# Kernel optimization log

Measured on AMD Instinct MI355X. Metric: run time of the kernel, lower is better.

The kernel has to match this reference:

```python
import jax, jax.numpy as jnp
import numpy as np

B, N, H = 32, 2048, 128


def _lstm_step(c, h, x, Wi, Wh, b):
    # flax LSTMCell: gates i,f,g,o; sigmoid/sigmoid/tanh/sigmoid
    gates = x @ Wi + h @ Wh + b  # (B,N,4H)
    i, f, g, o = jnp.split(gates, 4, axis=-1)
    c_new = jax.nn.sigmoid(f) * c + jax.nn.sigmoid(i) * jnp.tanh(g)
    h_new = jax.nn.sigmoid(o) * jnp.tanh(c_new)
    return c_new, h_new


def setup_inputs() -> dict:
    key = jax.random.key(0)
    ks = jax.random.split(key, 24)
    f32 = jnp.float32
    inp = {}
    inp['node_embeddings'] = jax.random.normal(ks[0], (B, N, H), f32)
    for nm, k in zip(['hs_c0', 'hs_h0', 'hs_c1', 'hs_h1'], ks[1:5]):
        inp[nm] = jax.random.normal(k, (B, N, H), f32)
    ip = jax.random.uniform(ks[5], (B, N), f32)
    inp['instruction_pointer'] = ip / jnp.sum(ip, axis=-1, keepdims=True)
    inp['Wi0'] = jax.random.normal(ks[6], (H, 4 * H), f32) * 0.05
    inp['Wh0'] = jax.random.normal(ks[7], (H, 4 * H), f32) * 0.05
    inp['b0'] = jnp.zeros((4 * H,), f32)
    inp['Wi1'] = jax.random.normal(ks[8], (H, 4 * H), f32) * 0.05
    inp['Wh1'] = jax.random.normal(ks[9], (H, 4 * H), f32) * 0.05
    inp['b1'] = jnp.zeros((4 * H,), f32)
    inp['W_raise'] = jax.random.normal(ks[10], (4 * H, 2), f32) * 0.05
    inp['b_raise'] = jnp.zeros((2,), f32)
    inp['W_branch'] = jax.random.normal(ks[11], (4 * H, 2), f32) * 0.05
    inp['b_branch'] = jnp.zeros((2,), f32)
    inp['true_indexes'] = jax.random.randint(ks[12], (B, N), 0, N, jnp.int32)
    inp['false_indexes'] = jax.random.randint(ks[13], (B, N), 0, N, jnp.int32)
    inp['raise_indexes'] = jax.random.randint(ks[14], (B, N), 0, N, jnp.int32)
    inp['exit_node_indexes'] = jax.random.randint(ks[15], (B,), 0, N, jnp.int32)
    inp['raise_node_indexes'] = jax.random.randint(ks[16], (B,), 0, N, jnp.int32)
    inp['step_limits'] = jax.random.randint(ks[17], (B,), 0, 100, jnp.int32)
    inp['current_step'] = 5
    return inp


def reference(node_embeddings, hs_c0, hs_h0, hs_c1, hs_h1, instruction_pointer,
              Wi0, Wh0, b0, Wi1, Wh1, b1, W_raise, b_raise, W_branch, b_branch,
              true_indexes, false_indexes, raise_indexes,
              exit_node_indexes, raise_node_indexes, step_limits, current_step):
    bidx = jnp.arange(B)
    old = [hs_c0, hs_h0, hs_c1, hs_h1]

    # execute: per-node 2-layer stacked LSTM (vectorized over B,N)
    c0n, h0n = _lstm_step(hs_c0, hs_h0, node_embeddings, Wi0, Wh0, b0)
    c1n, h1n = _lstm_step(hs_c1, hs_h1, h0n, Wi1, Wh1, b1)
    contrib = [c0n, h0n, c1n, h1n]

    # mask_h: keep old state at exit node and (raise_in_ipagnn) at raise node
    def mask_nodes(hc, ho, idx):
        return hc.at[bidx, idx].set(ho[bidx, idx])
    contrib = [mask_nodes(mask_nodes(hc, ho, exit_node_indexes), ho, raise_node_indexes)
               for hc, ho in zip(contrib, old)]

    hs_emb = jnp.concatenate(contrib, axis=-1)  # (B,N,4H)

    raise_dec = jax.nn.softmax(hs_emb @ W_raise + b_raise, axis=-1)
    zero_one = jnp.array([0.0, 1.0], dtype=raise_dec.dtype)
    raise_dec = raise_dec.at[bidx, exit_node_indexes].set(zero_one)
    raise_dec = raise_dec.at[bidx, raise_node_indexes].set(zero_one)
    branch_dec = jax.nn.softmax(hs_emb @ W_branch + b_branch, axis=-1)

    p_raise = raise_dec[..., 0]
    p_noraise = raise_dec[..., 1]
    p_true = p_noraise * branch_dec[..., 0]
    p_false = p_noraise * branch_dec[..., 1]

    seg = jax.vmap(lambda v, idx: jax.ops.segment_sum(v, idx, num_segments=N))
    ip = instruction_pointer
    ip_new = (seg(p_raise * ip, raise_indexes)
              + seg(p_true * ip, true_indexes)
              + seg(p_false * ip, false_indexes))  # (B,N)
    denom = (ip_new + 1e-7)[..., None]

    wr = (p_raise * ip)[..., None]
    wt = (p_true * ip)[..., None]
    wf = (p_false * ip)[..., None]

    def agg(h):
        return (seg(h * wr, raise_indexes) + seg(h * wt, true_indexes)
                + seg(h * wf, false_indexes)) / denom
    hs_new = [agg(h) for h in contrib]

    # keep_old_if_done
    not_done = (current_step < step_limits)  # (B,)
    hs_out = [jnp.where(not_done[:, None, None], hn, ho) for hn, ho in zip(hs_new, old)]
    ip_out = jnp.where(not_done[:, None], ip_new, ip)

    # pack carry: (c0,h0,c1,h1, instruction_pointer) -> (B,N,4H+1)
    return jnp.concatenate(hs_out + [ip_out[..., None]], axis=-1)
```

## Files before the change

### kernel.cpp

```cpp
#include <hip/hip_runtime.h>
#include <stdint.h>

#define BB 32
#define NN 2048
#define HH 128
#define BN (BB*NN)

typedef short v8s __attribute__((ext_vector_type(8)));
typedef float v4f __attribute__((ext_vector_type(4)));

__device__ __forceinline__ unsigned short f2b(float f){
  union { float f; unsigned int i; } v; v.f = f;
  unsigned int x = v.i;
  unsigned int r = x + 0x7FFFu + ((x >> 16) & 1u);
  return (unsigned short)(r >> 16);
}
__device__ __forceinline__ unsigned int pk2(float a, float b){
  return (unsigned int)f2b(a) | ((unsigned int)f2b(b) << 16);
}
__device__ __forceinline__ float b2f(unsigned int s){
  union { unsigned int i; float f; } v; v.i = s << 16; return v.f;
}
__device__ __forceinline__ float frcp(float x){ return __builtin_amdgcn_rcpf(x); }
__device__ __forceinline__ float fsigm(float x){ return frcp(1.0f + __expf(-x)); }
__device__ __forceinline__ float ftanh(float x){ return 1.0f - 2.0f*frcp(1.0f + __expf(2.0f*x)); }

__global__ void kswz(const float* __restrict__ Wi0, const float* __restrict__ Wh0,
                     const float* __restrict__ Wi1, const float* __restrict__ Wh1,
                     unsigned short* __restrict__ Bsw0, unsigned short* __restrict__ Bsw1){
  int bid = blockIdx.x;
  int layer = bid >> 8;
  int kc = (bid >> 5) & 7;
  int ct = bid & 31;
  int lane = threadIdx.x;
  const float* Wi = layer ? Wi1 : Wi0;
  const float* Wh = layer ? Wh1 : Wh0;
  unsigned short* dst = layer ? Bsw1 : Bsw0;
  int col = ct*16 + (lane & 15);
  int kbase = kc*32 + (lane >> 4)*8;
  size_t o = ((size_t)(kc*32 + ct)*64 + (size_t)lane)*8;
  #pragma unroll
  for (int j = 0; j < 8; j++){
    int k = kbase + j;
    dst[o + j] = f2b((k < 128) ? Wi[k*512 + col] : Wh[(k-128)*512 + col]);
  }
}

#define ROWSB 32
#define PA 264
#define PH 136

__global__ __launch_bounds__(512, 4) void klstm2(
    const float* __restrict__ ne,
    float* __restrict__ c0, float* __restrict__ h0,
    float* __restrict__ c1, float* __restrict__ h1,
    unsigned short* __restrict__ sc0, unsigned short* __restrict__ sh0,
    unsigned short* __restrict__ sc1, unsigned short* __restrict__ sh1,
    const unsigned short* __restrict__ Bsw0, const float* __restrict__ b0,
    const unsigned short* __restrict__ Bsw1, const float* __restrict__ b1,
    const int* __restrict__ exit_idx, const int* __restrict__ raise_idx,
    const int* __restrict__ step_limits, const int* __restrict__ cur_step,
    int useb)
{
  __shared__ unsigned short ldsA[ROWSB*PA];
  __shared__ unsigned short ldsH[ROWSB*PH];
  __shared__ unsigned short ldsG[ROWSB*PH];

  int rowbase = blockIdx.x * ROWSB;
  int b = rowbase >> 11;
  if (cur_step[0] >= step_limits[b]) return;

  int tid = threadIdx.x;
  int wid = tid >> 6, lane = tid & 63;
  int quad = lane >> 4, l16 = lane & 15;
  int ch = wid*16 + l16;
  int e_row = exit_idx[b], r_row = raise_idx[b];

  #pragma unroll
  for (int p = 0; p < 4; p++){
    int idx = p*512 + tid;
    int row = idx >> 6, chunk = idx & 63;
    size_t g = (size_t)(rowbase + row)*128 + (chunk & 31)*4;
    float4 v = (chunk < 32) ? *(const float4*)(ne + g) : *(const float4*)(h0 + g);
    uint2 w; w.x = pk2(v.x, v.y); w.y = pk2(v.z, v.w);
    *(uint2*)&ldsA[row*PA + chunk*4] = w;
  }
  __syncthreads();

  float cpre[8], bias[4];
  #pragma unroll
  for (int rt = 0; rt < 2; rt++)
    #pragma unroll
    for (int r = 0; r < 4; r++)
      cpre[rt*4+r] = c0[((size_t)rowbase + rt*16 + quad*4 + r)*128 + ch];
  #pragma unroll
  for (int g = 0; g < 4; g++) bias[g] = b0[g*128 + ch];

  #pragma unroll
  for (int p = 0; p < 2; p++){
    int idx = p*512 + tid;
    int row = idx >> 5, chunk = idx & 31;
    float4 v = *(const float4*)(h1 + (size_t)(rowbase + row)*128 + chunk*4);
    uint2 w; w.x = pk2(v.x, v.y); w.y = pk2(v.z, v.w);
    *(uint2*)&ldsH[row*PH + chunk*4] = w;
  }

  const v8s* Bv0 = (const v8s*)Bsw0;
  v4f acc[2][4] = {};
  v8s bc[4], bn[4];
  #pragma unroll
  for (int g = 0; g < 4; g++) bc[g] = Bv0[(size_t)(g*8 + wid)*64 + lane];
  #pragma unroll
  for (int kc = 0; kc < 8; kc++){
    if (kc < 7){
      #pragma unroll
      for (int g = 0; g < 4; g++) bn[g] = Bv0[(size_t)((kc+1)*32 + g*8 + wid)*64 + lane];
    }
    v8s a0 = *(const v8s*)&ldsA[(0*16 + l16)*PA + kc*32 + quad*8];
    v8s a1 = *(const v8s*)&ldsA[(1*16 + l16)*PA + kc*32 + quad*8];
    #pragma unroll
    for (int g = 0; g < 4; g++){
      acc[0][g] = __builtin_amdgcn_mfma_f32_16x16x32_bf16(a0, bc[g], acc[0][g], 0,0,0);
      acc[1][g] = __builtin_amdgcn_mfma_f32_16x16x32_bf16(a1, bc[g], acc[1][g], 0,0,0);
    }
    #pragma unroll
    for (int g = 0; g < 4; g++) bc[g] = bn[g];
  }

  #pragma unroll
  for (int rt = 0; rt < 2; rt++){
    #pragma unroll
    for (int r = 0; r < 4; r++){
      int k = rt*4 + r;
      int lrow = rt*16 + quad*4 + r;
      int grow = rowbase + lrow;
      int node = grow & 2047;
      bool special = (node == e_row) || (node == r_row);
      float iv = acc[rt][0][r] + bias[0];
      float fv = acc[rt][1][r] + bias[1];
      float gv = acc[rt][2][r] + bias[2];
      float ov = acc[rt][3][r] + bias[3];
      float cn = fsigm(fv)*cpre[k] + fsigm(iv)*ftanh(gv);
      float hn = fsigm(ov)*ftanh(cn);
      if (useb){
        sc0[(size_t)grow*128 + ch] = special ? f2b(cpre[k]) : f2b(cn);
        sh0[(size_t)grow*128 + ch] = special ? ldsA[lrow*PA + 128 + ch] : f2b(hn);
      } else if (!special){
        c0[(size_t)grow*128 + ch] = cn;
        h0[(size_t)grow*128 + ch] = hn;
      }
      ldsG[lrow*PH + ch] = f2b(hn);
    }
  }

  #pragma unroll
  for (int rt = 0; rt < 2; rt++)
    #pragma unroll
    for (int r = 0; r < 4; r++)
      cpre[rt*4+r] = c1[((size_t)rowbase + rt*16 + quad*4 + r)*128 + ch];
  #pragma unroll
  for (int g = 0; g < 4; g++) bias[g] = b1[g*128 + ch];
  const v8s* Bv1 = (const v8s*)Bsw1;
  #pragma unroll
  for (int g = 0; g < 4; g++) bc[g] = Bv1[(size_t)(g*8 + wid)*64 + lane];

  __syncthreads();

  #pragma unroll
  for (int rt = 0; rt < 2; rt++)
    #pragma unroll
    for (int g = 0; g < 4; g++)
      acc[rt][g] = (v4f){0.f, 0.f, 0.f, 0.f};
  #pragma unroll
  for (int kc = 0; kc < 8; kc++){
    if (kc < 7){
      #pragma unroll
      for (int g = 0; g < 4; g++) bn[g] = Bv1[(size_t)((kc+1)*32 + g*8 + wid)*64 + lane];
    }
    v8s a0, a1;
    if (kc < 4){
      a0 = *(const v8s*)&ldsG[(0*16 + l16)*PH + kc*32 + quad*8];
      a1 = *(const v8s*)&ldsG[(1*16 + l16)*PH + kc*32 + quad*8];
    } else {
      a0 = *(const v8s*)&ldsH[(0*16 + l16)*PH + (kc-4)*32 + quad*8];
      a1 = *(const v8s*)&ldsH[(1*16 + l16)*PH + (kc-4)*32 + quad*8];
    }
    #pragma unroll
    for (int g = 0; g < 4; g++){
      acc[0][g] = __builtin_amdgcn_mfma_f32_16x16x32_bf16(a0, bc[g], acc[0][g], 0,0,0);
      acc[1][g] = __builtin_amdgcn_mfma_f32_16x16x32_bf16(a1, bc[g], acc[1][g], 0,0,0);
    }
    #pragma unroll
    for (int g = 0; g < 4; g++) bc[g] = bn[g];
  }

  #pragma unroll
  for (int rt = 0; rt < 2; rt++){
    #pragma unroll
    for (int r = 0; r < 4; r++){
      int k = rt*4 + r;
      int lrow = rt*16 + quad*4 + r;
      int grow = rowbase + lrow;
      int node = grow & 2047;
      bool special = (node == e_row) || (node == r_row);
      float iv = acc[rt][0][r] + bias[0];
      float fv = acc[rt][1][r] + bias[1];
      float gv = acc[rt][2][r] + bias[2];
      float ov = acc[rt][3][r] + bias[3];
      float cn = fsigm(fv)*cpre[k] + fsigm(iv)*ftanh(gv);
      float hn = fsigm(ov)*ftanh(cn);
      if (useb){
        sc1[(size_t)grow*128 + ch] = special ? f2b(cpre[k]) : f2b(cn);
        sh1[(size_t)grow*128 + ch] = special ? ldsH[lrow*PH + ch] : f2b(hn);
      } else if (!special){
        c1[(size_t)grow*128 + ch] = cn;
        h1[(size_t)grow*128 + ch] = hn;
      }
    }
  }
}

__global__ __launch_bounds__(256) void kdec(
    const float* __restrict__ c0, const float* __restrict__ h0,
    const float* __restrict__ c1, const float* __restrict__ h1,
    const unsigned short* __restrict__ sc0, const unsigned short* __restrict__ sh0,
    const unsigned short* __restrict__ sc1, const unsigned short* __restrict__ sh1,
    const float* __restrict__ Wr, const float* __restrict__ br,
    const float* __restrict__ Wb, const float* __restrict__ bb,
    const float* __restrict__ ip,
    const int* __restrict__ exit_idx, const int* __restrict__ raise_idx,
    const int* __restrict__ ri, const int* __restrict__ ti, const int* __restrict__ fi,
    int* __restrict__ counts,
    float* __restrict__ wbuf, int useb)
{
  int tid = threadIdx.x;
  int wid = tid >> 6, lane = tid & 63;
  int gid = blockIdx.x*4 + wid;
  int b = gid >> 11, n = gid & 2047;

  float hv[8];
  if (useb){
    const unsigned short* bufs16[4] = {sc0, sh0, sc1, sh1};
    const unsigned short* hb = bufs16[lane >> 4] + (size_t)gid*128 + (lane & 15)*8;
    uint4 raw = *(const uint4*)hb;
    hv[0] = b2f(raw.x & 0xffffu); hv[1] = b2f(raw.x >> 16);
    hv[2] = b2f(raw.y & 0xffffu); hv[3] = b2f(raw.y >> 16);
    hv[4] = b2f(raw.z & 0xffffu); hv[5] = b2f(raw.z >> 16);
    hv[6] = b2f(raw.w & 0xffffu); hv[7] = b2f(raw.w >> 16);
  } else {
    const float* bufs[4] = {c0, h0, c1, h1};
    const float* hb = bufs[lane >> 4] + (size_t)gid*128 + (lane & 15)*8;
    float4 hv0 = *(const float4*)hb;
    float4 hv1 = *(const float4*)(hb + 4);
    hv[0]=hv0.x; hv[1]=hv0.y; hv[2]=hv0.z; hv[3]=hv0.w;
    hv[4]=hv1.x; hv[5]=hv1.y; hv[6]=hv1.z; hv[7]=hv1.w;
  }
  const float* wrp = Wr + lane*16;
  const float* wbp = Wb + lane*16;
  float r0=0.f, r1=0.f, q0=0.f, q1=0.f;
  #pragma unroll
  for (int j = 0; j < 8; j++){
    float h = hv[j];
    r0 += h * wrp[j*2];  r1 += h * wrp[j*2+1];
    q0 += h * wbp[j*2];  q1 += h * wbp[j*2+1];
  }
  #pragma unroll
  for (int off = 32; off > 0; off >>= 1){
    r0 += __shfl_xor(r0, off, 64);
    r1 += __shfl_xor(r1, off, 64);
    q0 += __shfl_xor(q0, off, 64);
    q1 += __shfl_xor(q1, off, 64);
  }
  if (lane == 0){
    r0 += br[0]; r1 += br[1];
    q0 += bb[0]; q1 += bb[1];
    float pr, pn;
    if (n == exit_idx[b] || n == raise_idx[b]){ pr = 0.f; pn = 1.f; }
    else {
      float m = fmaxf(r0, r1);
      float e0 = __expf(r0 - m), e1 = __expf(r1 - m);
      pr = e0 / (e0 + e1); pn = e1 / (e0 + e1);
    }
    float m2 = fmaxf(q0, q1);
    float f0 = __expf(q0 - m2), f1 = __expf(q1 - m2);
    float pt = f0 / (f0 + f1), pf = f1 / (f0 + f1);
    float ipv = ip[gid];
    wbuf[0*BN + gid] = pr * ipv;
    wbuf[1*BN + gid] = pn * pt * ipv;
    wbuf[2*BN + gid] = pn * pf * ipv;
  } else if (lane == 1){
    atomicAdd(&counts[(b<<11) + ri[gid]], 1);
  } else if (lane == 2){
    atomicAdd(&counts[(b<<11) + ti[gid]], 1);
  } else if (lane == 3){
    atomicAdd(&counts[(b<<11) + fi[gid]], 1);
  }
}

__global__ __launch_bounds__(256) void kscan(const int* __restrict__ counts,
                                             int* __restrict__ offsets,
                                             int* __restrict__ cursor){
  __shared__ int lds[256];
  int b = blockIdx.x, tid = threadIdx.x;
  const int* c = counts + b*NN;
  int* o = offsets + b*NN;
  int* cu = cursor + b*NN;
  int v[8]; int s = 0;
  #pragma unroll
  for (int i = 0; i < 8; i++){ v[i] = c[tid*8+i]; s += v[i]; cu[tid*8+i] = 0; }
  lds[tid] = s;
  __syncthreads();
  if (tid == 0){
    int run = 0;
    for (int t = 0; t < 256; t++){ int tmp = lds[t]; lds[t] = run; run += tmp; }
  }
  __syncthreads();
  int off = lds[tid];
  #pragma unroll
  for (int i = 0; i < 8; i++){ o[tid*8+i] = off; off += v[i]; }
}

__global__ void kfill(const int* __restrict__ ri, const int* __restrict__ ti,
                      const int* __restrict__ fi, const int* __restrict__ offsets,
                      int* __restrict__ cursor, unsigned short* __restrict__ edges){
  int gid = blockIdx.x*256 + threadIdx.x;
  int b = gid >> 11, n = gid & 2047;
  size_t ebase = (size_t)b*3*NN;
  int t0 = ri[gid]; int p0 = atomicAdd(&cursor[b*NN+t0], 1);
  edges[ebase + offsets[b*NN+t0] + p0] = (unsigned short)(n);
  int t1 = ti[gid]; int p1 = atomicAdd(&cursor[b*NN+t1], 1);
  edges[ebase + offsets[b*NN+t1] + p1] = (unsigned short)(n | (1<<11));
  int t2 = fi[gid]; int p2 = atomicAdd(&cursor[b*NN+t2], 1);
  edges[ebase + offsets[b*NN+t2] + p2] = (unsigned short)(n | (2<<11));
}

__global__ __launch_bounds__(128) void kagg(
    const float* __restrict__ c0, const float* __restrict__ h0,
    const float* __restrict__ c1, const float* __restrict__ h1,
    const unsigned short* __restrict__ sc0, const unsigned short* __restrict__ sh0,
    const unsigned short* __restrict__ sc1, const unsigned short* __restrict__ sh1,
    const float* __restrict__ ip,
    const float* __restrict__ wbuf, const unsigned short* __restrict__ edges,
    const int* __restrict__ counts, const int* __restrict__ offsets,
    const int* __restrict__ step_limits, const int* __restrict__ cur_step,
    float* __restrict__ out, int useb)
{
  int gid = blockIdx.x;
  int b = gid >> 11;
  int tid = threadIdx.x;
  size_t obase = (size_t)gid*513;
  const float* bufs[4] = {c0, h0, c1, h1};

  if (cur_step[0] >= step_limits[b]){
    int c = tid*4;
    const float* s = bufs[c >> 7];
    size_t rb = (size_t)gid*128 + (c & 127);
    out[obase + c+0] = s[rb+0];
    out[obase + c+1] = s[rb+1];
    out[obase + c+2] = s[rb+2];
    out[obase + c+3] = s[rb+3];
    if (tid == 0) out[obase + 512] = ip[gid];
    return;
  }

  int cnt = counts[gid], off = offsets[gid];
  const unsigned short* eb = edges + (size_t)b*3*NN + off;
  int coff = (tid & 31)*4;
  float a0=0.f, a1=0.f, a2=0.f, a3=0.f, ipn=0.f;
  int pk = (cnt > 0) ? eb[0] : 0;
  if (useb){
    const unsigned short* bufs16[4] = {sc0, sh0, sc1, sh1};
    const unsigned short* sb = bufs16[tid >> 5];
    for (int e = 0; e < cnt; e++){
      int pkn = (e+1 < cnt) ? eb[e+1] : 0;
      int n = pk & 2047, et = pk >> 11;
      float w = wbuf[et*BN + (b<<11) + n];
      uint2 raw = *(const uint2*)(sb + ((size_t)(b<<11) + n)*128 + coff);
      ipn += w;
      a0 += w * b2f(raw.x & 0xffffu);
      a1 += w * b2f(raw.x >> 16);
      a2 += w * b2f(raw.y & 0xffffu);
      a3 += w * b2f(raw.y >> 16);
      pk = pkn;
    }
  } else {
    const float* sb = bufs[tid >> 5];
    for (int e = 0; e < cnt; e++){
      int pkn = (e+1 < cnt) ? eb[e+1] : 0;
      int n = pk & 2047, et = pk >> 11;
      float w = wbuf[et*BN + (b<<11) + n];
      float4 sv = *(const float4*)(sb + ((size_t)(b<<11) + n)*128 + coff);
      ipn += w;
      a0 += w * sv.x;
      a1 += w * sv.y;
      a2 += w * sv.z;
      a3 += w * sv.w;
      pk = pkn;
    }
  }
  int c = tid*4;
  float inv = 1.0f / (ipn + 1e-7f);
  out[obase + c+0] = a0*inv;
  out[obase + c+1] = a1*inv;
  out[obase + c+2] = a2*inv;
  out[obase + c+3] = a3*inv;
  if (tid == 0) out[obase + 512] = ipn;
}

extern "C" void kernel_launch(void* const* d_in, const int* in_sizes, int n_in,
                              void* d_out, int out_size, void* d_ws, size_t ws_size,
                              hipStream_t stream){
  const float* ne  = (const float*)d_in[0];
  float* c0  = (float*)d_in[1];
  float* h0  = (float*)d_in[2];
  float* c1  = (float*)d_in[3];
  float* h1  = (float*)d_in[4];
  const float* ip  = (const float*)d_in[5];
  const float* Wi0 = (const float*)d_in[6];
  const float* Wh0 = (const float*)d_in[7];
  const float* b0  = (const float*)d_in[8];
  const float* Wi1 = (const float*)d_in[9];
  const float* Wh1 = (const float*)d_in[10];
  const float* b1  = (const float*)d_in[11];
  const float* Wr  = (const float*)d_in[12];
  const float* br  = (const float*)d_in[13];
  const float* Wb  = (const float*)d_in[14];
  const float* bb  = (const float*)d_in[15];
  const int* ti  = (const int*)d_in[16];
  const int* fi  = (const int*)d_in[17];
  const int* ri  = (const int*)d_in[18];
  const int* ei  = (const int*)d_in[19];
  const int* rni = (const int*)d_in[20];
  const int* sl  = (const int*)d_in[21];
  const int* cs  = (const int*)d_in[22];
  float* out = (float*)d_out;

  uint8_t* ws = (uint8_t*)d_ws;
  unsigned short* Bsw0    = (unsigned short*)(ws + 0);
  unsigned short* Bsw1    = (unsigned short*)(ws + 262144);
  float*          wbuf    = (float*)(ws + 655360);
  int*            counts  = (int*)(ws + 1441792);
  int*            offsets = (int*)(ws + 1703936);
  int*            cursor  = (int*)(ws + 1966080);
  unsigned short* edges   = (unsigned short*)(ws + 2228224);
  const size_t SBASE = 2621440;
  const size_t SB    = (size_t)BN * 128 * 2;
  int useb = (ws_size >= SBASE + 4*SB) ? 1 : 0;
  unsigned short* sc0 = (unsigned short*)(ws + SBASE + 0*SB);
  unsigned short* sh0 = (unsigned short*)(ws + SBASE + 1*SB);
  unsigned short* sc1 = (unsigned short*)(ws + SBASE + 2*SB);
  unsigned short* sh1 = (unsigned short*)(ws + SBASE + 3*SB);

  hipMemsetAsync(counts, 0, BN*sizeof(int), stream);

  kswz<<<512, 64, 0, stream>>>(Wi0, Wh0, Wi1, Wh1, Bsw0, Bsw1);

  klstm2<<<BN/ROWSB, 512, 0, stream>>>(ne, c0, h0, c1, h1,
                                       sc0, sh0, sc1, sh1,
                                       Bsw0, b0, Bsw1, b1,
                                       ei, rni, sl, cs, useb);

  kdec<<<BN/4, 256, 0, stream>>>(c0, h0, c1, h1, sc0, sh0, sc1, sh1,
                                 Wr, br, Wb, bb, ip, ei, rni,
                                 ri, ti, fi, counts, wbuf, useb);

  kscan<<<BB, 256, 0, stream>>>(counts, offsets, cursor);
  kfill<<<BN/256, 256, 0, stream>>>(ri, ti, fi, offsets, cursor, edges);

  kagg<<<BN, 128, 0, stream>>>(c0, h0, c1, h1, sc0, sh0, sc1, sh1,
                               ip, wbuf, edges, counts, offsets,
                               sl, cs, out, useb);
}
```

Baseline: 441.4 us.

## Build CSR edge lists per batch in one LDS kernel and pack kagg blocks

Replaces the global-atomic count, the scan and fill kernels, and the counts memset with a single per-batch kernel that counts, scans and fills the edge lists using shared-memory atomics. This removes two launches, a memset and global atomic traffic from kdec. The CSR kernel runs only 32 blocks, which may be slow on its own, but it does not depend on the LSTM output and is placed before it. kagg now handles four nodes per 512-thread block instead of one node per 128-thread block, cutting the block count. The kagg body may contain __syncthreads or shared-memory use that was written for a single node per block, which is a correctness risk.

```diff
diff --git a/kernel.cpp b/kernel.cpp
--- a/kernel.cpp
+++ b/kernel.cpp
@@ -229,8 +229,6 @@
     const float* __restrict__ Wb, const float* __restrict__ bb,
     const float* __restrict__ ip,
     const int* __restrict__ exit_idx, const int* __restrict__ raise_idx,
-    const int* __restrict__ ri, const int* __restrict__ ti, const int* __restrict__ fi,
-    int* __restrict__ counts,
     float* __restrict__ wbuf, int useb)
 {
   int tid = threadIdx.x;
@@ -288,53 +286,80 @@
     wbuf[0*BN + gid] = pr * ipv;
     wbuf[1*BN + gid] = pn * pt * ipv;
     wbuf[2*BN + gid] = pn * pf * ipv;
-  } else if (lane == 1){
-    atomicAdd(&counts[(b<<11) + ri[gid]], 1);
-  } else if (lane == 2){
-    atomicAdd(&counts[(b<<11) + ti[gid]], 1);
-  } else if (lane == 3){
-    atomicAdd(&counts[(b<<11) + fi[gid]], 1);
-  }
-}
-
-__global__ __launch_bounds__(256) void kscan(const int* __restrict__ counts,
-                                             int* __restrict__ offsets,
-                                             int* __restrict__ cursor){
-  __shared__ int lds[256];
+  }
+}
+
+__global__ __launch_bounds__(1024) void kcsr(
+    const int* __restrict__ ri, const int* __restrict__ ti,
+    const int* __restrict__ fi,
+    int* __restrict__ counts, int* __restrict__ offsets,
+    unsigned short* __restrict__ edges)
+{
+  __shared__ int cnt[NN];
+  __shared__ int off[NN];
+  __shared__ int cur[NN];
+  __shared__ int wpart[16];
+
   int b = blockIdx.x, tid = threadIdx.x;
-  const int* c = counts + b*NN;
-  int* o = offsets + b*NN;
-  int* cu = cursor + b*NN;
-  int v[8]; int s = 0;
-  #pragma unroll
-  for (int i = 0; i < 8; i++){ v[i] = c[tid*8+i]; s += v[i]; cu[tid*8+i] = 0; }
-  lds[tid] = s;
+  const int* rp = ri + b*NN;
+  const int* tp = ti + b*NN;
+  const int* fp = fi + b*NN;
+
+  #pragma unroll
+  for (int p = 0; p < 2; p++){ cnt[p*1024 + tid] = 0; cur[p*1024 + tid] = 0; }
+  __syncthreads();
+
+  int rv[2], tv[2], fv[2];
+  #pragma unroll
+  for (int p = 0; p < 2; p++){
+    int n = p*1024 + tid;
+    rv[p] = rp[n]; tv[p] = tp[n]; fv[p] = fp[n];
+    atomicAdd(&cnt[rv[p]], 1);
+    atomicAdd(&cnt[tv[p]], 1);
+    atomicAdd(&cnt[fv[p]], 1);
+  }
+  __syncthreads();
+
+  int c0 = cnt[2*tid], c1 = cnt[2*tid+1];
+  int s = c0 + c1;
+  int lane = tid & 63, wv = tid >> 6;
+  int inc = s;
+  #pragma unroll
+  for (int d = 1; d < 64; d <<= 1){
+    int t = __shfl_up(inc, d, 64);
+    if (lane >= d) inc += t;
+  }
+  if (lane == 63) wpart[wv] = inc;
   __syncthreads();
   if (tid == 0){
     int run = 0;
-    for (int t = 0; t < 256; t++){ int tmp = lds[t]; lds[t] = run; run += tmp; }
-  }
-  __syncthreads();
-  int off = lds[tid];
-  #pragma unroll
-  for (int i = 0; i < 8; i++){ o[tid*8+i] = off; off += v[i]; }
-}
-
-__global__ void kfill(const int* __restrict__ ri, const int* __restrict__ ti,
-                      const int* __restrict__ fi, const int* __restrict__ offsets,
-                      int* __restrict__ cursor, unsigned short* __restrict__ edges){
-  int gid = blockIdx.x*256 + threadIdx.x;
-  int b = gid >> 11, n = gid & 2047;
+    #pragma unroll
+    for (int w = 0; w < 16; w++){ int t = wpart[w]; wpart[w] = run; run += t; }
+  }
+  __syncthreads();
+  int excl = wpart[wv] + inc - s;
+  off[2*tid]   = excl;
+  off[2*tid+1] = excl + c0;
+  offsets[b*NN + 2*tid]   = excl;
+  offsets[b*NN + 2*tid+1] = excl + c0;
+  counts[b*NN + 2*tid]   = c0;
+  counts[b*NN + 2*tid+1] = c1;
+  __syncthreads();
+
   size_t ebase = (size_t)b*3*NN;
-  int t0 = ri[gid]; int p0 = atomicAdd(&cursor[b*NN+t0], 1);
-  edges[ebase + offsets[b*NN+t0] + p0] = (unsigned short)(n);
-  int t1 = ti[gid]; int p1 = atomicAdd(&cursor[b*NN+t1], 1);
-  edges[ebase + offsets[b*NN+t1] + p1] = (unsigned short)(n | (1<<11));
-  int t2 = fi[gid]; int p2 = atomicAdd(&cursor[b*NN+t2], 1);
-  edges[ebase + offsets[b*NN+t2] + p2] = (unsigned short)(n | (2<<11));
-}
-
-__global__ __launch_bounds__(128) void kagg(
+  #pragma unroll
+  for (int p = 0; p < 2; p++){
+    int n = p*1024 + tid;
+    int t0 = rv[p]; int p0 = atomicAdd(&cur[t0], 1);
+    edges[ebase + off[t0] + p0] = (unsigned short)n;
+    int t1 = tv[p]; int p1 = atomicAdd(&cur[t1], 1);
+    edges[ebase + off[t1] + p1] = (unsigned short)(n | (1<<11));
+    int t2 = fv[p]; int p2 = atomicAdd(&cur[t2], 1);
+    edges[ebase + off[t2] + p2] = (unsigned short)(n | (2<<11));
+  }
+}
+
+__global__ __launch_bounds__(512) void kagg(
     const float* __restrict__ c0, const float* __restrict__ h0,
     const float* __restrict__ c1, const float* __restrict__ h1,
     const unsigned short* __restrict__ sc0, const unsigned short* __restrict__ sh0,
@@ -345,9 +370,11 @@
     const int* __restrict__ step_limits, const int* __restrict__ cur_step,
     float* __restrict__ out, int useb)
 {
-  int gid = blockIdx.x;
+  int tid0 = threadIdx.x;
+  int sub = tid0 >> 7;
+  int tid = tid0 & 127;
+  int gid = blockIdx.x*4 + sub;
   int b = gid >> 11;
-  int tid = threadIdx.x;
   size_t obase = (size_t)gid*513;
   const float* bufs[4] = {c0, h0, c1, h1};
 
@@ -441,7 +468,6 @@
   float*          wbuf    = (float*)(ws + 655360);
   int*            counts  = (int*)(ws + 1441792);
   int*            offsets = (int*)(ws + 1703936);
-  int*            cursor  = (int*)(ws + 1966080);
   unsigned short* edges   = (unsigned short*)(ws + 2228224);
   const size_t SBASE = 2621440;
   const size_t SB    = (size_t)BN * 128 * 2;
@@ -451,9 +477,9 @@
   unsigned short* sc1 = (unsigned short*)(ws + SBASE + 2*SB);
   unsigned short* sh1 = (unsigned short*)(ws + SBASE + 3*SB);
 
-  hipMemsetAsync(counts, 0, BN*sizeof(int), stream);
-
   kswz<<<512, 64, 0, stream>>>(Wi0, Wh0, Wi1, Wh1, Bsw0, Bsw1);
+
+  kcsr<<<BB, 1024, 0, stream>>>(ri, ti, fi, counts, offsets, edges);
 
   klstm2<<<BN/ROWSB, 512, 0, stream>>>(ne, c0, h0, c1, h1,
                                        sc0, sh0, sc1, sh1,
@@ -461,13 +487,9 @@
                                        ei, rni, sl, cs, useb);
 
   kdec<<<BN/4, 256, 0, stream>>>(c0, h0, c1, h1, sc0, sh0, sc1, sh1,
-                                 Wr, br, Wb, bb, ip, ei, rni,
-                                 ri, ti, fi, counts, wbuf, useb);
-
-  kscan<<<BB, 256, 0, stream>>>(counts, offsets, cursor);
-  kfill<<<BN/256, 256, 0, stream>>>(ri, ti, fi, offsets, cursor, edges);
-
-  kagg<<<BN, 128, 0, stream>>>(c0, h0, c1, h1, sc0, sh0, sc1, sh1,
-                               ip, wbuf, edges, counts, offsets,
-                               sl, cs, out, useb);
-}
+                                 Wr, br, Wb, bb, ip, ei, rni, wbuf, useb);
+
+  kagg<<<BN/4, 512, 0, stream>>>(c0, h0, c1, h1, sc0, sh0, sc1, sh1,
+                                 ip, wbuf, edges, counts, offsets,
+                                 sl, cs, out, useb);
+}
```

Result: faster. 425.3 us (-3.7%).
